# Performance work log

Hardware: AMD Instinct MI355X
Metric: run time of the kernel (lower is better)

Reference implementation:

```python
import jax, jax.numpy as jnp
import numpy as np

B, S, HID = 2, 2048, 4096
H, KVH, D = 32, 8, 128
THETA = 10000.0
SCALE = D ** -0.5


def _rope(x, positions):
    # x: [B, S, nH, D], positions: [B, S] int. Neox style: rotate halves.
    half = D // 2
    inv_freq = 1.0 / (THETA ** (jnp.arange(0, half, dtype=jnp.float32) / half))
    ang = positions.astype(jnp.float32)[..., None] * inv_freq  # [B,S,half]
    cos = jnp.cos(ang)[:, :, None, :]  # [B,S,1,half]
    sin = jnp.sin(ang)[:, :, None, :]
    x1, x2 = x[..., :half], x[..., half:]
    return jnp.concatenate([x1 * cos - x2 * sin, x2 * cos + x1 * sin], axis=-1)


def setup_inputs() -> dict:
    key = jax.random.key(0)
    k1, k2, k3, k4, k5 = jax.random.split(key, 5)
    std_in = HID ** -0.5
    return {
        "positions": jnp.tile(jnp.arange(S, dtype=jnp.int32), (B, 1)),
        "hidden_states": jax.random.normal(k1, (B, S, HID), jnp.float32),
        "wq": jax.random.normal(k2, (HID, H * D), jnp.float32) * std_in,
        "wk": jax.random.normal(k3, (HID, KVH * D), jnp.float32) * std_in,
        "wv": jax.random.normal(k4, (HID, KVH * D), jnp.float32) * std_in,
        "wo": jax.random.normal(k5, (H * D, HID), jnp.float32) * ((H * D) ** -0.5),
    }


def reference(positions, hidden_states, wq, wk, wv, wo):
    # Separate Q/K/V projections (bias=False)
    q = (hidden_states @ wq).reshape(B, S, H, D)
    k = (hidden_states @ wk).reshape(B, S, KVH, D)
    v = (hidden_states @ wv).reshape(B, S, KVH, D)
    # RoPE on q and k
    q = _rope(q, positions)
    k = _rope(k, positions)
    # GQA: expand KV heads to query heads
    group = H // KVH
    k = jnp.repeat(k, group, axis=2)  # [B,S,H,D]
    v = jnp.repeat(v, group, axis=2)
    # Causal scaled dot-product attention
    scores = jnp.einsum("bqhd,bkhd->bhqk", q, k) * SCALE
    causal = jnp.tril(jnp.ones((S, S), dtype=bool))
    scores = jnp.where(causal, scores, jnp.finfo(scores.dtype).min)
    probs = jax.nn.softmax(scores, axis=-1)
    attn = jnp.einsum("bhqk,bkhd->bqhd", probs, v).reshape(B, S, H * D)
    return attn @ wo
```

## Files before the change

### kernel.cpp

```cpp
#include <hip/hip_runtime.h>
#include <cstdint>

typedef __bf16 bf16;
typedef __attribute__((ext_vector_type(4))) __bf16 bf16x4;
typedef __attribute__((ext_vector_type(8))) __bf16 bf16x8;
typedef __attribute__((ext_vector_type(4))) float f32x4;

#define DEVI __device__ __forceinline__

#define BATCH 2
#define SEQ 2048
#define HID 4096
#define NH 32
#define NKVH 8
#define HD 128
#define QKVN 6144
#define MROWS 4096
#define ATT_SCALE 0.08838834764831845f
#define QSCALE (0.08838834764831845f * 1.4426950408889634f)

DEVI void gload_lds16(const bf16* g, bf16* l) {
  __builtin_amdgcn_global_load_lds(
      (__attribute__((address_space(1))) void*)(g),
      (__attribute__((address_space(3))) void*)(l), 16, 0, 0);
}

__global__ void h2b_kernel(const float* __restrict__ in, bf16* __restrict__ out) {
  long i = ((long)blockIdx.x * 256 + threadIdx.x) * 4;
  float4 v = *(const float4*)(in + i);
  bf16x4 o;
  o[0] = (bf16)v.x; o[1] = (bf16)v.y; o[2] = (bf16)v.z; o[3] = (bf16)v.w;
  *(bf16x4*)(out + i) = o;
}

__global__ void wtrans_kernel(const float* __restrict__ in, bf16* __restrict__ out,
                              int K, int N) {
  __shared__ float t[32][33];
  int n0 = blockIdx.x * 32, k0 = blockIdx.y * 32;
  int tx = threadIdx.x, ty = threadIdx.y;
#pragma unroll
  for (int r = 0; r < 4; ++r) {
    int k = ty + r * 8;
    t[k][tx] = in[(long)(k0 + k) * N + n0 + tx];
  }
  __syncthreads();
#pragma unroll
  for (int r = 0; r < 4; ++r) {
    int n = ty + r * 8;
    out[(long)(n0 + n) * K + k0 + tx] = (bf16)t[tx][n];
  }
}

__global__ void rope_kernel(bf16* __restrict__ qkv, const int* __restrict__ pos) {
  long idx = (long)blockIdx.x * 256 + threadIdx.x;
  if (idx >= (long)MROWS * 40 * 64) return;
  int d = idx & 63;
  long t = idx >> 6;
  int hh = (int)(t % 40);
  int row = (int)(t / 40);
  int colb = hh < NH ? hh * HD : NH * HD + (hh - NH) * HD;
  float p = (float)pos[row];
  float inv_freq = exp2f((float)d * -0.2076205059304601f);
  float ang = p * inv_freq;
  float sn = sinf(ang), cs = cosf(ang);
  bf16* base = qkv + (long)row * QKVN + colb + d;
  float x1 = (float)base[0], x2 = (float)base[64];
  base[0] = (bf16)(x1 * cs - x2 * sn);
  base[64] = (bf16)(x2 * cs + x1 * sn);
}

__global__ void vtrans_kernel(const bf16* __restrict__ qkv, bf16* __restrict__ vt) {
  __shared__ bf16 t[32][33];
  int s0 = blockIdx.x * 32, d0 = blockIdx.y * 32, bk = blockIdx.z;
  int b = bk >> 3, kvh = bk & 7;
  int tx = threadIdx.x, ty = threadIdx.y;
#pragma unroll
  for (int r = 0; r < 4; ++r) {
    int s = ty + r * 8;
    t[s][tx] = qkv[(long)(b * SEQ + s0 + s) * QKVN + 5120 + kvh * HD + d0 + tx];
  }
  __syncthreads();
#pragma unroll
  for (int r = 0; r < 4; ++r) {
    int d = ty + r * 8;
    vt[((long)bk * HD + d0 + d) * SEQ + s0 + tx] = t[tx][d];
  }
}

template <typename OutT>
__global__ __launch_bounds__(512, 2)
void gemm8p(const bf16* __restrict__ A, const bf16* __restrict__ BT,
            OutT* __restrict__ C, int M, int N, int K) {
  extern __shared__ __align__(16) bf16 lds[];
  const int tid = threadIdx.x;
  const int lane = tid & 63, wave = tid >> 6;
  const int wm = wave >> 2, wn = wave & 3;
  const int l16 = lane & 15, lhi = lane >> 4;
  const int nwg = gridDim.x * gridDim.y;
  const int bid = blockIdx.y * gridDim.x + blockIdx.x;
  const int cpx = nwg >> 3;
  const int swz = (bid & 7) * cpx + (bid >> 3);
  const int bx = swz % gridDim.x, by = swz / gridDim.x;
  const long bm0 = (long)by * 256, bn0 = (long)bx * 256;

  bf16* Alds = lds;
  bf16* Blds = lds + 32768;
  const int NT = K >> 6;

  f32x4 acc[8][4] = {};

  auto stageH = [&](const bf16* src, long row0, long k0, bf16* dst) {
#pragma unroll
    for (int j = 0; j < 2; ++j) {
      int r = j * 64 + (tid >> 3);
      int sc = (tid & 7) ^ (r & 7);
      gload_lds16(src + (row0 + r) * (long)K + k0 + sc * 8,
                  dst + j * 4096 + tid * 8);
    }
  };

  stageH(A, bm0, 0, Alds);
  stageH(A, bm0 + 128, 0, Alds + 8192);
  stageH(BT, bn0, 0, Blds);
  stageH(BT, bn0 + 128, 0, Blds + 8192);
  {
    long k1 = (NT > 1) ? 64 : 0;
    stageH(BT, bn0, k1, Blds + 16384);
    stageH(BT, bn0 + 128, k1, Blds + 24576);
    stageH(A, bm0, k1, Alds + 16384);
  }
  asm volatile("s_waitcnt vmcnt(6)" ::: "memory");
  __builtin_amdgcn_s_barrier();
  __builtin_amdgcn_sched_barrier(0);

  const int arow0 = wm * 128 + l16;
  const int brow0 = wn * 64 + l16;

  for (int t = 0; t < NT; ++t) {
    const bf16* Ab = Alds + (t & 1) * 16384;
    const bf16* Bb = Blds + (t & 1) * 16384;
    bf16* A1 = Alds + ((t + 1) & 1) * 16384;
    bf16* A2 = Alds + (t & 1) * 16384;
    bf16* B2 = Blds + (t & 1) * 16384;
    const long k1 = (long)((t + 1 < NT) ? t + 1 : NT - 1) << 6;
    const long k2 = (long)((t + 2 < NT) ? t + 2 : NT - 1) << 6;

    bf16x8 a0[4][2], a1r[4][2], b0[2][2], b1[2][2];
#pragma unroll
    for (int i = 0; i < 4; ++i) {
      int mr = arow0 + i * 16;
#pragma unroll
      for (int kk = 0; kk < 2; ++kk)
        a0[i][kk] = *(const bf16x8*)(Ab + mr * 64 + (((kk * 4 + lhi) ^ (mr & 7))) * 8);
    }
#pragma unroll
    for (int n = 0; n < 2; ++n) {
      int br = brow0 + n * 16;
#pragma unroll
      for (int kk = 0; kk < 2; ++kk)
        b0[n][kk] = *(const bf16x8*)(Bb + br * 64 + (((kk * 4 + lhi) ^ (br & 7))) * 8);
    }
    stageH(A, bm0 + 128, k1, A1 + 8192);
    __builtin_amdgcn_sched_barrier(0);
    __builtin_amdgcn_s_barrier();
    __builtin_amdgcn_sched_barrier(0);
    __builtin_amdgcn_s_setprio(1);
#pragma unroll
    for (int i = 0; i < 4; ++i)
#pragma unroll
      for (int n = 0; n < 2; ++n)
#pragma unroll
        for (int kk = 0; kk < 2; ++kk)
          acc[i][n] = __builtin_amdgcn_mfma_f32_16x16x32_bf16(a0[i][kk], b0[n][kk], acc[i][n], 0, 0, 0);
    __builtin_amdgcn_s_setprio(0);
    __builtin_amdgcn_sched_barrier(0);
    __builtin_amdgcn_s_barrier();
#pragma unroll
    for (int n = 0; n < 2; ++n) {
      int br = brow0 + (n + 2) * 16;
#pragma unroll
      for (int kk = 0; kk < 2; ++kk)
        b1[n][kk] = *(const bf16x8*)(Bb + br * 64 + (((kk * 4 + lhi) ^ (br & 7))) * 8);
    }
    __builtin_amdgcn_sched_barrier(0);
    __builtin_amdgcn_s_barrier();
    __builtin_amdgcn_sched_barrier(0);
    __builtin_amdgcn_s_setprio(1);
#pragma unroll
    for (int i = 0; i < 4; ++i)
#pragma unroll
      for (int n = 0; n < 2; ++n)
#pragma unroll
        for (int kk = 0; kk < 2; ++kk)
          acc[i][n + 2] = __builtin_amdgcn_mfma_f32_16x16x32_bf16(a0[i][kk], b1[n][kk], acc[i][n + 2], 0, 0, 0);
    __builtin_amdgcn_s_setprio(0);
    __builtin_amdgcn_sched_barrier(0);
    __builtin_amdgcn_s_barrier();
#pragma unroll
    for (int i = 0; i < 4; ++i) {
      int mr = arow0 + 64 + i * 16;
#pragma unroll
      for (int kk = 0; kk < 2; ++kk)
        a1r[i][kk] = *(const bf16x8*)(Ab + mr * 64 + (((kk * 4 + lhi) ^ (mr & 7))) * 8);
    }
    stageH(BT, bn0, k2, B2);
    __builtin_amdgcn_sched_barrier(0);
    __builtin_amdgcn_s_barrier();
    __builtin_amdgcn_sched_barrier(0);
    __builtin_amdgcn_s_setprio(1);
#pragma unroll
    for (int i = 0; i < 4; ++i)
#pragma unroll
      for (int n = 0; n < 2; ++n)
#pragma unroll
        for (int kk = 0; kk < 2; ++kk)
          acc[4 + i][n + 2] = __builtin_amdgcn_mfma_f32_16x16x32_bf16(a1r[i][kk], b1[n][kk], acc[4 + i][n + 2], 0, 0, 0);
    __builtin_amdgcn_s_setprio(0);
    __builtin_amdgcn_sched_barrier(0);
    __builtin_amdgcn_s_barrier();
    stageH(BT, bn0 + 128, k2, B2 + 8192);
    stageH(A, bm0, k2, A2);
    __builtin_amdgcn_sched_barrier(0);
    __builtin_amdgcn_s_barrier();
    __builtin_amdgcn_sched_barrier(0);
    __builtin_amdgcn_s_setprio(1);
#pragma unroll
    for (int i = 0; i < 4; ++i)
#pragma unroll
      for (int n = 0; n < 2; ++n)
#pragma unroll
        for (int kk = 0; kk < 2; ++kk)
          acc[4 + i][n] = __builtin_amdgcn_mfma_f32_16x16x32_bf16(a1r[i][kk], b0[n][kk], acc[4 + i][n], 0, 0, 0);
    __builtin_amdgcn_s_setprio(0);
    __builtin_amdgcn_sched_barrier(0);
    asm volatile("s_waitcnt vmcnt(6)" ::: "memory");
    __builtin_amdgcn_s_barrier();
    __builtin_amdgcn_sched_barrier(0);
  }
  asm volatile("s_waitcnt vmcnt(0)" ::: "memory");
#pragma unroll
  for (int mi = 0; mi < 8; ++mi)
#pragma unroll
    for (int r = 0; r < 4; ++r) {
      long grow = bm0 + wm * 128 + mi * 16 + lhi * 4 + r;
#pragma unroll
      for (int n = 0; n < 4; ++n) {
        long gcol = bn0 + wn * 64 + n * 16 + l16;
        C[grow * N + gcol] = (OutT)acc[mi][n][r];
      }
    }
}

__global__ __launch_bounds__(512, 4)
void attn_kernel(const bf16* __restrict__ qkv, const bf16* __restrict__ vt,
                 bf16* __restrict__ out) {
  extern __shared__ __align__(16) bf16 smem[];
  const int pi = blockIdx.x, h = blockIdx.y, b = blockIdx.z;
  const int kvh = h >> 2;
  const int tid = threadIdx.x, lane = tid & 63, wave = tid >> 6;
  const int l16 = lane & 15, lhi = lane >> 4;
  const int kloc = lhi * 4;
  bf16* Pw = smem + 32768 + wave * 1024;

  const bf16* kpan = qkv + (long)(b * SEQ) * QKVN + 4096 + kvh * HD;
  const bf16* vpan = vt + (long)(b * NKVH + kvh) * HD * SEQ;

  auto stageKV = [&](int buf, int step) {
    const int kv0 = step * 64;
    bf16* kd = smem + buf * 8192;
    bf16* vd = smem + 16384 + buf * 8192;
#pragma unroll
    for (int i = 0; i < 2; ++i) {
      int kr = wave * 8 + i * 4 + lhi;
      gload_lds16(kpan + (long)(kv0 + kr) * QKVN + (l16 ^ (kr & 7)) * 8,
                  kd + (wave * 8 + i * 4) * 128);
      int vr = wave * 16 + i * 8 + (lane >> 3);
      gload_lds16(vpan + (long)vr * SEQ + kv0 + ((lane & 7) ^ (vr & 7)) * 8,
                  vd + (wave * 16 + i * 8) * 64);
    }
  };

  auto process_chunk = [&](int q0, int nsteps) {
    bf16x8 qf[4];
    const bf16* qb = qkv + (long)(b * SEQ + q0 + wave * 16 + l16) * QKVN + h * HD + lhi * 8;
#pragma unroll
    for (int di = 0; di < 4; ++di) {
      bf16x8 raw = *(const bf16x8*)(qb + di * 32);
      bf16x8 sc;
#pragma unroll
      for (int j = 0; j < 8; ++j) sc[j] = (bf16)((float)raw[j] * QSCALE);
      qf[di] = sc;
    }
    f32x4 oacc[8] = {};
    float m_run = -1e30f, l_run = 0.f;
    const int qg = q0 + wave * 16 + l16;

    stageKV(0, 0);
    __syncthreads();

    for (int step = 0; step < nsteps; ++step) {
      const int kv0 = step * 64;
      const int cur = step & 1;
      if (step + 1 < nsteps) stageKV(cur ^ 1, step + 1);
      const bf16* Kc = smem + cur * 8192;
      const bf16* Vc = smem + 16384 + cur * 8192;

      f32x4 s[4];
      __builtin_amdgcn_s_setprio(1);
#pragma unroll
      for (int c = 0; c < 4; ++c) {
        s[c] = (f32x4){0.f, 0.f, 0.f, 0.f};
        int kr = c * 16 + l16;
#pragma unroll
        for (int di = 0; di < 4; ++di) {
          bf16x8 kf = *(const bf16x8*)(Kc + kr * 128 + (((di * 4 + lhi) ^ (kr & 7))) * 8);
          s[c] = __builtin_amdgcn_mfma_f32_16x16x32_bf16(kf, qf[di], s[c], 0, 0, 0);
        }
      }
      __builtin_amdgcn_s_setprio(0);
#pragma unroll
      for (int c = 0; c < 4; ++c)
#pragma unroll
        for (int r = 0; r < 4; ++r) {
          int kcol = kv0 + c * 16 + kloc + r;
          if (kcol > qg) s[c][r] = -1e30f;
        }
      float mloc = s[0][0];
#pragma unroll
      for (int c = 0; c < 4; ++c)
#pragma unroll
        for (int r = 0; r < 4; ++r) mloc = fmaxf(mloc, s[c][r]);
      mloc = fmaxf(mloc, __shfl_xor(mloc, 16, 64));
      mloc = fmaxf(mloc, __shfl_xor(mloc, 32, 64));
      bool skip = __all(mloc - m_run <= 8.0f);
      float alpha = 1.f;
      if (!skip) {
        float mn = fmaxf(m_run, mloc);
        alpha = exp2f(m_run - mn);
        m_run = mn;
      }
      float sm = 0.f;
      bf16x4 pb[4];
#pragma unroll
      for (int c = 0; c < 4; ++c)
#pragma unroll
        for (int r = 0; r < 4; ++r) {
          float p = exp2f(s[c][r] - m_run);
          sm += p;
          pb[c][r] = (bf16)p;
        }
      sm += __shfl_xor(sm, 16, 64);
      sm += __shfl_xor(sm, 32, 64);
      l_run = l_run * alpha + sm;
#pragma unroll
      for (int c = 0; c < 4; ++c) {
        int sl = (c * 2 + (lhi >> 1)) ^ (l16 & 7);
        *(bf16x4*)(Pw + l16 * 64 + sl * 8 + (lhi & 1) * 4) = pb[c];
      }
      if (!skip) {
        float a_o[4];
#pragma unroll
        for (int r = 0; r < 4; ++r) a_o[r] = __shfl(alpha, kloc + r, 64);
#pragma unroll
        for (int dj = 0; dj < 8; ++dj)
#pragma unroll
          for (int r = 0; r < 4; ++r) oacc[dj][r] *= a_o[r];
      }
      __builtin_amdgcn_s_setprio(1);
#pragma unroll
      for (int kh = 0; kh < 2; ++kh) {
        bf16x8 pf = *(const bf16x8*)(Pw + l16 * 64 + (((kh * 4 + lhi) ^ (l16 & 7))) * 8);
#pragma unroll
        for (int dj = 0; dj < 8; ++dj) {
          int vr = dj * 16 + l16;
          bf16x8 vf = *(const bf16x8*)(Vc + vr * 64 + (((kh * 4 + lhi) ^ (vr & 7))) * 8);
          oacc[dj] = __builtin_amdgcn_mfma_f32_16x16x32_bf16(pf, vf, oacc[dj], 0, 0, 0);
        }
      }
      __builtin_amdgcn_s_setprio(0);
      __syncthreads();
    }
    float linv[4];
#pragma unroll
    for (int r = 0; r < 4; ++r) linv[r] = 1.f / __shfl(l_run, kloc + r, 64);
#pragma unroll
    for (int r = 0; r < 4; ++r) {
      long orow = (long)(b * SEQ + q0 + wave * 16 + lhi * 4 + r);
#pragma unroll
      for (int dj = 0; dj < 8; ++dj)
        out[orow * (NH * HD) + h * HD + dj * 16 + l16] = (bf16)(oacc[dj][r] * linv[r]);
    }
  };

  process_chunk(pi * 128, 2 * pi + 2);
  process_chunk((15 - pi) * 128, 32 - 2 * pi);
}

extern "C" void kernel_launch(void* const* d_in, const int* in_sizes, int n_in,
                              void* d_out, int out_size, void* d_ws, size_t ws_size,
                              hipStream_t stream) {
  const int* positions = (const int*)d_in[0];
  const float* hidden = (const float*)d_in[1];
  const float* wq = (const float*)d_in[2];
  const float* wk = (const float*)d_in[3];
  const float* wv = (const float*)d_in[4];
  const float* wo = (const float*)d_in[5];
  float* out = (float*)d_out;
  char* ws = (char*)d_ws;

  const size_t SZ_H = (size_t)MROWS * HID * 2;
  const size_t SZ_WQKV = (size_t)QKVN * HID * 2;
  const size_t SZ_WO = (size_t)HID * HID * 2;
  bf16* h_bf = (bf16*)(ws);
  bf16* wqkvT = (bf16*)(ws + SZ_H);
  bf16* woT = (bf16*)(ws + SZ_H + SZ_WQKV);
  bf16* qkv = (bf16*)(ws + SZ_H + SZ_WQKV + SZ_WO);
  bf16* attn = h_bf;
  bf16* vtbuf = wqkvT;

  const int GEMM_SMEM = 131072;
  const int ATTN_SMEM = 40960 * 2;
  auto* g1 = gemm8p<bf16>;
  auto* g2 = gemm8p<float>;
  hipFuncSetAttribute(reinterpret_cast<const void*>(g1),
                      hipFuncAttributeMaxDynamicSharedMemorySize, GEMM_SMEM);
  hipFuncSetAttribute(reinterpret_cast<const void*>(g2),
                      hipFuncAttributeMaxDynamicSharedMemorySize, GEMM_SMEM);
  hipFuncSetAttribute(reinterpret_cast<const void*>(attn_kernel),
                      hipFuncAttributeMaxDynamicSharedMemorySize, ATTN_SMEM);

  h2b_kernel<<<(MROWS * (long)HID) / (256 * 4), 256, 0, stream>>>(hidden, h_bf);
  dim3 t32(32, 8);
  wtrans_kernel<<<dim3(HID / 32, HID / 32), t32, 0, stream>>>(wq, wqkvT, HID, HID);
  wtrans_kernel<<<dim3(1024 / 32, HID / 32), t32, 0, stream>>>(wk, wqkvT + (long)4096 * HID, HID, 1024);
  wtrans_kernel<<<dim3(1024 / 32, HID / 32), t32, 0, stream>>>(wv, wqkvT + (long)5120 * HID, HID, 1024);
  wtrans_kernel<<<dim3(HID / 32, HID / 32), t32, 0, stream>>>(wo, woT, HID, HID);
  gemm8p<bf16><<<dim3(QKVN / 256, MROWS / 256), 512, GEMM_SMEM, stream>>>(h_bf, wqkvT, qkv, MROWS, QKVN, HID);
  rope_kernel<<<(MROWS * 40 * 64) / 256, 256, 0, stream>>>(qkv, positions);
  vtrans_kernel<<<dim3(SEQ / 32, HD / 32, BATCH * NKVH), t32, 0, stream>>>(qkv, vtbuf);
  attn_kernel<<<dim3(8, NH, BATCH), 512, ATTN_SMEM, stream>>>(qkv, vtbuf, attn);
  gemm8p<float><<<dim3(HID / 256, MROWS / 256), 512, GEMM_SMEM, stream>>>(attn, woT, out, MROWS, HID, HID);
}
```

Measured before the change: 553.3 us.

## Add triple-buffered 256x128 GEMM for output projection, reorder gemm8p phases, vectorize RoPE

Introduces a new gemm256 kernel with 256x128 tiles and a three-slot LDS ring buffer, used for the output projection in place of gemm8p. The goal is more workgroups for better CU fill and simpler load/compute overlap. The gemm8p main loop is reordered so A rows are consumed before B halves, with explicit lgkmcnt waits and fewer sched barriers. RoPE now processes 8 elements per thread with vector loads and fast __sincosf, which can lose some accuracy in the angle computation for large positions.

```diff
diff --git a/kernel.cpp b/kernel.cpp
--- a/kernel.cpp
+++ b/kernel.cpp
@@ -52,21 +52,29 @@
 }
 
 __global__ void rope_kernel(bf16* __restrict__ qkv, const int* __restrict__ pos) {
-  long idx = (long)blockIdx.x * 256 + threadIdx.x;
-  if (idx >= (long)MROWS * 40 * 64) return;
-  int d = idx & 63;
-  long t = idx >> 6;
-  int hh = (int)(t % 40);
-  int row = (int)(t / 40);
+  long t = (long)blockIdx.x * 256 + threadIdx.x;
+  int d8 = (int)(t & 7) * 8;
+  long u = t >> 3;
+  int hh = (int)(u % 40);
+  int row = (int)(u / 40);
   int colb = hh < NH ? hh * HD : NH * HD + (hh - NH) * HD;
   float p = (float)pos[row];
-  float inv_freq = exp2f((float)d * -0.2076205059304601f);
-  float ang = p * inv_freq;
-  float sn = sinf(ang), cs = cosf(ang);
-  bf16* base = qkv + (long)row * QKVN + colb + d;
-  float x1 = (float)base[0], x2 = (float)base[64];
-  base[0] = (bf16)(x1 * cs - x2 * sn);
-  base[64] = (bf16)(x2 * cs + x1 * sn);
+  bf16* base = qkv + (long)row * QKVN + colb + d8;
+  bf16x8 x1v = *(const bf16x8*)(base);
+  bf16x8 x2v = *(const bf16x8*)(base + 64);
+  bf16x8 o1, o2;
+#pragma unroll
+  for (int j = 0; j < 8; ++j) {
+    float inv_freq = exp2f((float)(d8 + j) * -0.2076205059304601f);
+    float ang = p * inv_freq;
+    float sn, cs;
+    __sincosf(ang, &sn, &cs);
+    float x1 = (float)x1v[j], x2 = (float)x2v[j];
+    o1[j] = (bf16)(x1 * cs - x2 * sn);
+    o2[j] = (bf16)(x2 * cs + x1 * sn);
+  }
+  *(bf16x8*)(base) = o1;
+  *(bf16x8*)(base + 64) = o2;
 }
 
 __global__ void vtrans_kernel(const bf16* __restrict__ qkv, bf16* __restrict__ vt) {
@@ -85,6 +93,89 @@
     int d = ty + r * 8;
     vt[((long)bk * HD + d0 + d) * SEQ + s0 + tx] = t[tx][d];
   }
+}
+
+template <typename OutT>
+__global__ __launch_bounds__(512, 2)
+void gemm256(const bf16* __restrict__ A, const bf16* __restrict__ BT,
+             OutT* __restrict__ C, int M, int N, int K) {
+  extern __shared__ __align__(16) bf16 lds[];
+  const int tid = threadIdx.x;
+  const int lane = tid & 63, wave = tid >> 6;
+  const int wm = wave >> 1, wn = wave & 1;
+  const int l16 = lane & 15, lhi = lane >> 4;
+  const int nwg = gridDim.x * gridDim.y;
+  const int bid = blockIdx.y * gridDim.x + blockIdx.x;
+  const int cpx = nwg >> 3;
+  const int swz = (bid & 7) * cpx + (bid >> 3);
+  const int bx = swz % gridDim.x, by = swz / gridDim.x;
+  const long bm0 = (long)by * 256, bn0 = (long)bx * 128;
+
+  const int srow8 = lane >> 3;
+  const int scol = (lane & 7) ^ srow8;
+
+  const int NT = K >> 6;
+  f32x4 acc[4][4] = {};
+
+  auto stage = [&](int slot, int t) {
+    const long k0 = (long)t << 6;
+    bf16* dst = lds + slot * 24576;
+#pragma unroll
+    for (int i = 0; i < 4; ++i) {
+      int r = (wave * 4 + i) * 8 + srow8;
+      gload_lds16(A + (bm0 + r) * K + k0 + scol * 8,
+                  dst + (wave * 4 + i) * 512 + lane * 8);
+    }
+#pragma unroll
+    for (int i = 0; i < 2; ++i) {
+      int r = (wave * 2 + i) * 8 + srow8;
+      gload_lds16(BT + (bn0 + r) * K + k0 + scol * 8,
+                  dst + 16384 + (wave * 2 + i) * 512 + lane * 8);
+    }
+  };
+
+  stage(0, 0);
+  stage(1, 1);
+
+  for (int t = 0; t < NT; ++t) {
+    asm volatile("s_waitcnt vmcnt(6)" ::: "memory");
+    __builtin_amdgcn_s_barrier();
+    __builtin_amdgcn_sched_barrier(0);
+    const int nxt = (t + 2 < NT) ? t + 2 : NT - 1;
+    stage((t + 2) % 3, nxt);
+    const bf16* As = lds + (t % 3) * 24576;
+    const bf16* Bs = As + 16384;
+#pragma unroll
+    for (int kk = 0; kk < 2; ++kk) {
+      bf16x8 af[4], bw[4];
+#pragma unroll
+      for (int i = 0; i < 4; ++i) {
+        int ar = wm * 64 + i * 16 + l16;
+        af[i] = *(const bf16x8*)(As + ar * 64 + (((kk * 4 + lhi) ^ (ar & 7))) * 8);
+        int br = wn * 64 + i * 16 + l16;
+        bw[i] = *(const bf16x8*)(Bs + br * 64 + (((kk * 4 + lhi) ^ (br & 7))) * 8);
+      }
+      __builtin_amdgcn_s_setprio(1);
+#pragma unroll
+      for (int i = 0; i < 4; ++i)
+#pragma unroll
+        for (int j = 0; j < 4; ++j)
+          acc[i][j] = __builtin_amdgcn_mfma_f32_16x16x32_bf16(af[i], bw[j], acc[i][j], 0, 0, 0);
+      __builtin_amdgcn_s_setprio(0);
+    }
+  }
+  asm volatile("s_waitcnt vmcnt(0)" ::: "memory");
+#pragma unroll
+  for (int i = 0; i < 4; ++i)
+#pragma unroll
+    for (int r = 0; r < 4; ++r) {
+      long grow = bm0 + wm * 64 + i * 16 + lhi * 4 + r;
+#pragma unroll
+      for (int j = 0; j < 4; ++j) {
+        long gcol = bn0 + wn * 64 + j * 16 + l16;
+        C[grow * N + gcol] = (OutT)acc[i][j][r];
+      }
+    }
 }
 
 template <typename OutT>
@@ -124,14 +215,13 @@
   stageH(BT, bn0, 0, Blds);
   stageH(BT, bn0 + 128, 0, Blds + 8192);
   {
-    long k1 = (NT > 1) ? 64 : 0;
-    stageH(BT, bn0, k1, Blds + 16384);
-    stageH(BT, bn0 + 128, k1, Blds + 24576);
-    stageH(A, bm0, k1, Alds + 16384);
+    long k1p = (NT > 1) ? 64 : 0;
+    stageH(A, bm0, k1p, Alds + 16384);
+    stageH(BT, bn0, k1p, Blds + 16384);
+    stageH(BT, bn0 + 128, k1p, Blds + 24576);
   }
   asm volatile("s_waitcnt vmcnt(6)" ::: "memory");
   __builtin_amdgcn_s_barrier();
-  __builtin_amdgcn_sched_barrier(0);
 
   const int arow0 = wm * 128 + l16;
   const int brow0 = wn * 64 + l16;
@@ -139,13 +229,13 @@
   for (int t = 0; t < NT; ++t) {
     const bf16* Ab = Alds + (t & 1) * 16384;
     const bf16* Bb = Blds + (t & 1) * 16384;
-    bf16* A1 = Alds + ((t + 1) & 1) * 16384;
-    bf16* A2 = Alds + (t & 1) * 16384;
-    bf16* B2 = Blds + (t & 1) * 16384;
+    bf16* Aopp = Alds + ((t + 1) & 1) * 16384;
+    bf16* Asame = Alds + (t & 1) * 16384;
+    bf16* Bsame = Blds + (t & 1) * 16384;
     const long k1 = (long)((t + 1 < NT) ? t + 1 : NT - 1) << 6;
     const long k2 = (long)((t + 2 < NT) ? t + 2 : NT - 1) << 6;
 
-    bf16x8 a0[4][2], a1r[4][2], b0[2][2], b1[2][2];
+    bf16x8 a0[4][2], a1[4][2], b0[2][2], b1[2][2];
 #pragma unroll
     for (int i = 0; i < 4; ++i) {
       int mr = arow0 + i * 16;
@@ -160,9 +250,8 @@
       for (int kk = 0; kk < 2; ++kk)
         b0[n][kk] = *(const bf16x8*)(Bb + br * 64 + (((kk * 4 + lhi) ^ (br & 7))) * 8);
     }
-    stageH(A, bm0 + 128, k1, A1 + 8192);
-    __builtin_amdgcn_sched_barrier(0);
-    __builtin_amdgcn_s_barrier();
+    __builtin_amdgcn_s_barrier();
+    asm volatile("s_waitcnt lgkmcnt(0)" ::: "memory");
     __builtin_amdgcn_sched_barrier(0);
     __builtin_amdgcn_s_setprio(1);
 #pragma unroll
@@ -173,7 +262,27 @@
         for (int kk = 0; kk < 2; ++kk)
           acc[i][n] = __builtin_amdgcn_mfma_f32_16x16x32_bf16(a0[i][kk], b0[n][kk], acc[i][n], 0, 0, 0);
     __builtin_amdgcn_s_setprio(0);
+    __builtin_amdgcn_s_barrier();
+#pragma unroll
+    for (int i = 0; i < 4; ++i) {
+      int mr = arow0 + 64 + i * 16;
+#pragma unroll
+      for (int kk = 0; kk < 2; ++kk)
+        a1[i][kk] = *(const bf16x8*)(Ab + mr * 64 + (((kk * 4 + lhi) ^ (mr & 7))) * 8);
+    }
+    stageH(A, bm0 + 128, k1, Aopp + 8192);
+    __builtin_amdgcn_s_barrier();
+    asm volatile("s_waitcnt lgkmcnt(0)" ::: "memory");
     __builtin_amdgcn_sched_barrier(0);
+    __builtin_amdgcn_s_setprio(1);
+#pragma unroll
+    for (int i = 0; i < 4; ++i)
+#pragma unroll
+      for (int n = 0; n < 2; ++n)
+#pragma unroll
+        for (int kk = 0; kk < 2; ++kk)
+          acc[4 + i][n] = __builtin_amdgcn_mfma_f32_16x16x32_bf16(a1[i][kk], b0[n][kk], acc[4 + i][n], 0, 0, 0);
+    __builtin_amdgcn_s_setprio(0);
     __builtin_amdgcn_s_barrier();
 #pragma unroll
     for (int n = 0; n < 2; ++n) {
@@ -182,9 +291,23 @@
       for (int kk = 0; kk < 2; ++kk)
         b1[n][kk] = *(const bf16x8*)(Bb + br * 64 + (((kk * 4 + lhi) ^ (br & 7))) * 8);
     }
+    stageH(A, bm0, k2, Asame);
+    __builtin_amdgcn_s_barrier();
+    asm volatile("s_waitcnt lgkmcnt(0)" ::: "memory");
     __builtin_amdgcn_sched_barrier(0);
-    __builtin_amdgcn_s_barrier();
-    __builtin_amdgcn_sched_barrier(0);
+    __builtin_amdgcn_s_setprio(1);
+#pragma unroll
+    for (int i = 0; i < 4; ++i)
+#pragma unroll
+      for (int n = 0; n < 2; ++n)
+#pragma unroll
+        for (int kk = 0; kk < 2; ++kk)
+          acc[4 + i][n + 2] = __builtin_amdgcn_mfma_f32_16x16x32_bf16(a1[i][kk], b1[n][kk], acc[4 + i][n + 2], 0, 0, 0);
+    __builtin_amdgcn_s_setprio(0);
+    __builtin_amdgcn_s_barrier();
+    stageH(BT, bn0, k2, Bsame);
+    stageH(BT, bn0 + 128, k2, Bsame + 8192);
+    __builtin_amdgcn_s_barrier();
     __builtin_amdgcn_s_setprio(1);
 #pragma unroll
     for (int i = 0; i < 4; ++i)
@@ -194,48 +317,8 @@
         for (int kk = 0; kk < 2; ++kk)
           acc[i][n + 2] = __builtin_amdgcn_mfma_f32_16x16x32_bf16(a0[i][kk], b1[n][kk], acc[i][n + 2], 0, 0, 0);
     __builtin_amdgcn_s_setprio(0);
-    __builtin_amdgcn_sched_barrier(0);
-    __builtin_amdgcn_s_barrier();
-#pragma unroll
-    for (int i = 0; i < 4; ++i) {
-      int mr = arow0 + 64 + i * 16;
-#pragma unroll
-      for (int kk = 0; kk < 2; ++kk)
-        a1r[i][kk] = *(const bf16x8*)(Ab + mr * 64 + (((kk * 4 + lhi) ^ (mr & 7))) * 8);
-    }
-    stageH(BT, bn0, k2, B2);
-    __builtin_amdgcn_sched_barrier(0);
-    __builtin_amdgcn_s_barrier();
-    __builtin_amdgcn_sched_barrier(0);
-    __builtin_amdgcn_s_setprio(1);
-#pragma unroll
-    for (int i = 0; i < 4; ++i)
-#pragma unroll
-      for (int n = 0; n < 2; ++n)
-#pragma unroll
-        for (int kk = 0; kk < 2; ++kk)
-          acc[4 + i][n + 2] = __builtin_amdgcn_mfma_f32_16x16x32_bf16(a1r[i][kk], b1[n][kk], acc[4 + i][n + 2], 0, 0, 0);
-    __builtin_amdgcn_s_setprio(0);
-    __builtin_amdgcn_sched_barrier(0);
-    __builtin_amdgcn_s_barrier();
-    stageH(BT, bn0 + 128, k2, B2 + 8192);
-    stageH(A, bm0, k2, A2);
-    __builtin_amdgcn_sched_barrier(0);
-    __builtin_amdgcn_s_barrier();
-    __builtin_amdgcn_sched_barrier(0);
-    __builtin_amdgcn_s_setprio(1);
-#pragma unroll
-    for (int i = 0; i < 4; ++i)
-#pragma unroll
-      for (int n = 0; n < 2; ++n)
-#pragma unroll
-        for (int kk = 0; kk < 2; ++kk)
-          acc[4 + i][n] = __builtin_amdgcn_mfma_f32_16x16x32_bf16(a1r[i][kk], b0[n][kk], acc[4 + i][n], 0, 0, 0);
-    __builtin_amdgcn_s_setprio(0);
-    __builtin_amdgcn_sched_barrier(0);
     asm volatile("s_waitcnt vmcnt(6)" ::: "memory");
     __builtin_amdgcn_s_barrier();
-    __builtin_amdgcn_sched_barrier(0);
   }
   asm volatile("s_waitcnt vmcnt(0)" ::: "memory");
 #pragma unroll
@@ -418,14 +501,15 @@
   bf16* attn = h_bf;
   bf16* vtbuf = wqkvT;
 
-  const int GEMM_SMEM = 131072;
+  const int G8P_SMEM = 131072;
+  const int R3_SMEM = 3 * 24576 * 2;
   const int ATTN_SMEM = 40960 * 2;
   auto* g1 = gemm8p<bf16>;
-  auto* g2 = gemm8p<float>;
+  auto* g2 = gemm256<float>;
   hipFuncSetAttribute(reinterpret_cast<const void*>(g1),
-                      hipFuncAttributeMaxDynamicSharedMemorySize, GEMM_SMEM);
+                      hipFuncAttributeMaxDynamicSharedMemorySize, G8P_SMEM);
   hipFuncSetAttribute(reinterpret_cast<const void*>(g2),
-                      hipFuncAttributeMaxDynamicSharedMemorySize, GEMM_SMEM);
+                      hipFuncAttributeMaxDynamicSharedMemorySize, R3_SMEM);
   hipFuncSetAttribute(reinterpret_cast<const void*>(attn_kernel),
                       hipFuncAttributeMaxDynamicSharedMemorySize, ATTN_SMEM);
 
@@ -435,9 +519,9 @@
   wtrans_kernel<<<dim3(1024 / 32, HID / 32), t32, 0, stream>>>(wk, wqkvT + (long)4096 * HID, HID, 1024);
   wtrans_kernel<<<dim3(1024 / 32, HID / 32), t32, 0, stream>>>(wv, wqkvT + (long)5120 * HID, HID, 1024);
   wtrans_kernel<<<dim3(HID / 32, HID / 32), t32, 0, stream>>>(wo, woT, HID, HID);
-  gemm8p<bf16><<<dim3(QKVN / 256, MROWS / 256), 512, GEMM_SMEM, stream>>>(h_bf, wqkvT, qkv, MROWS, QKVN, HID);
-  rope_kernel<<<(MROWS * 40 * 64) / 256, 256, 0, stream>>>(qkv, positions);
+  gemm8p<bf16><<<dim3(QKVN / 256, MROWS / 256), 512, G8P_SMEM, stream>>>(h_bf, wqkvT, qkv, MROWS, QKVN, HID);
+  rope_kernel<<<(MROWS * 40 * 8) / 256, 256, 0, stream>>>(qkv, positions);
   vtrans_kernel<<<dim3(SEQ / 32, HD / 32, BATCH * NKVH), t32, 0, stream>>>(qkv, vtbuf);
   attn_kernel<<<dim3(8, NH, BATCH), 512, ATTN_SMEM, stream>>>(qkv, vtbuf, attn);
-  gemm8p<float><<<dim3(HID / 256, MROWS / 256), 512, GEMM_SMEM, stream>>>(attn, woT, out, MROWS, HID, HID);
-}
+  gemm256<float><<<dim3(HID / 128, MROWS / 256), 512, R3_SMEM, stream>>>(attn, woT, out, MROWS, HID, HID);
+}
```

After: 561.5 us. About the same (+1.5%).
